# Kernel optimization log

Hardware: AMD Instinct MI355X
Metric: run time of the kernel (lower is better)

The kernel has to match this reference:

```python
import jax, jax.numpy as jnp
import numpy as np

B, H_, W_, C, HEADS, WS, SR = 4, 56, 56, 256, 8, 3, 4
HD = C // HEADS
N = H_ * W_
LL = WS * WS
PH, PW = H_ // SR, W_ // SR
PL = PH * PW
K_TAB = 2048


def _unfold3(x, H, W):
    # x: (B, C, H, W) -> (B, C, 9, H*W); matches torch nn.Unfold(kernel_size=3, padding=1)
    xp = jnp.pad(x, ((0, 0), (0, 0), (1, 1), (1, 1)))
    pats = jnp.stack([xp[:, :, i:i + H, j:j + W] for i in range(3) for j in range(3)], axis=2)
    return pats.reshape(x.shape[0], x.shape[1], 9, H * W)


def _l2n(x):
    # torch F.normalize(dim=-1) with eps=1e-12
    return x / jnp.maximum(jnp.linalg.norm(x, axis=-1, keepdims=True), 1e-12)


def setup_inputs() -> dict:
    key = jax.random.key(0)
    ks = jax.random.split(key, 24)
    x = jax.random.normal(ks[0], (B, N, C), jnp.float32)
    # padding mask from unfold of ones image (True where window element falls outside)
    ones = np.zeros((H_ + 2, W_ + 2), np.float32)
    ones[1:-1, 1:-1] = 1.0
    pats = np.stack([ones[i:i + H_, j:j + W_] for i in range(3) for j in range(3)], 0).reshape(9, N)
    padding_mask = jnp.asarray((pats == 0).T)  # (N, 9) bool
    local_valid = LL - padding_mask.sum(-1)
    seq_length_scale = jnp.log(local_valid.astype(jnp.float32) + PL)[:, None]  # (N,1)
    relative_pos_index = jax.random.randint(ks[1], (N * PL,), 0, K_TAB)
    relative_coords_table = jax.random.uniform(ks[2], (K_TAB, 2), jnp.float32, -1.0, 1.0)
    w = lambda k, shape: jax.random.normal(k, shape, jnp.float32) * 0.02
    inp = dict(
        x=x, H=H_, W=W_,
        relative_pos_index=relative_pos_index,
        relative_coords_table=relative_coords_table,
        seq_length_scale=seq_length_scale,
        padding_mask=padding_mask,
        q_w=w(ks[3], (C, C)), q_b=jnp.zeros((C,), jnp.float32),
        kv_w=w(ks[4], (2 * C, C)), kv_b=jnp.zeros((2 * C,), jnp.float32),
        sr_w=w(ks[5], (C, C)), sr_b=jnp.zeros((C,), jnp.float32),
        norm_g=jnp.ones((C,), jnp.float32), norm_b=jnp.zeros((C,), jnp.float32),
        cpb1_w=w(ks[6], (512, 2)), cpb1_b=jnp.zeros((512,), jnp.float32),
        cpb2_w=w(ks[7], (HEADS, 512)), cpb2_b=jnp.zeros((HEADS,), jnp.float32),
        temperature=jnp.log(jnp.exp(jnp.ones((HEADS, 1, 1), jnp.float32) / 0.24) - 1.0),
        query_embedding=w(ks[8], (HEADS, 1, HD)),
        rel_pos_bias_local=jax.random.normal(ks[9], (HEADS, LL), jnp.float32) * 0.0004,
        learnable_tokens=w(ks[10], (HEADS, HD, LL)),
        learnable_bias=jnp.zeros((HEADS, 1, LL), jnp.float32),
        proj_w=w(ks[11], (C, C)), proj_b=jnp.zeros((C,), jnp.float32),
    )
    return inp


def reference(x, H, W, relative_pos_index, relative_coords_table, seq_length_scale,
              padding_mask, q_w, q_b, kv_w, kv_b, sr_w, sr_b, norm_g, norm_b,
              cpb1_w, cpb1_b, cpb2_w, cpb2_b, temperature, query_embedding,
              rel_pos_bias_local, learnable_tokens, learnable_bias, proj_w, proj_b):
    Bsz, n, Cd = x.shape
    h, hd, ll = HEADS, HD, LL
    pH, pW = H // SR, W // SR
    pL = pH * pW
    # ----- queries -----
    q = (x @ q_w.T + q_b).reshape(Bsz, n, h, hd).transpose(0, 2, 1, 3)  # (B,h,N,d)
    q_norm = _l2n(q)
    q_scaled = (q_norm + query_embedding) * jax.nn.softplus(temperature) * seq_length_scale
    # ----- local branch: unfolded window KV -----
    kv = x @ kv_w.T + kv_b  # (B,N,2C)
    k_loc, v_loc = jnp.split(kv, 2, axis=-1)
    k_loc = _l2n(k_loc.reshape(Bsz, n, h, hd)).reshape(Bsz, n, Cd)
    kv_img = jnp.concatenate([k_loc, v_loc], -1).transpose(0, 2, 1).reshape(Bsz, 2 * Cd, H, W)
    pats = _unfold3(kv_img, H, W).reshape(Bsz, 2 * h, hd, ll, n).transpose(0, 1, 4, 2, 3)  # (B,2h,N,d,ll)
    k_local, v_local = jnp.split(pats, 2, axis=1)
    attn_local = jnp.einsum('bhnd,bhndl->bhnl', q_scaled, k_local) + rel_pos_bias_local[:, None, :]
    attn_local = jnp.where(padding_mask, -jnp.inf, attn_local)
    # ----- global branch: 1x1 conv -> GELU -> avg pool -> LN -> KV -----
    x_img = x.transpose(0, 2, 1).reshape(Bsz, Cd, H, W)
    x_sr = jax.nn.gelu(jnp.einsum('oc,bchw->bohw', sr_w, x_img) + sr_b[None, :, None, None], approximate=False)
    x_pool = x_sr.reshape(Bsz, Cd, pH, SR, pW, SR).mean(axis=(3, 5)).reshape(Bsz, Cd, pL).transpose(0, 2, 1)
    mu = x_pool.mean(-1, keepdims=True)
    var = x_pool.var(-1, keepdims=True)
    x_pool = (x_pool - mu) / jnp.sqrt(var + 1e-5) * norm_g + norm_b
    kvp = (x_pool @ kv_w.T + kv_b).reshape(Bsz, pL, 2 * h, hd).transpose(0, 2, 1, 3)
    k_pool, v_pool = jnp.split(kvp, 2, axis=1)  # each (B,h,pL,d)
    # CPB-MLP relative position bias (interpolate is identity since test==trained resolution)
    tab = jax.nn.relu(relative_coords_table @ cpb1_w.T + cpb1_b) @ cpb2_w.T + cpb2_b  # (K,h)
    pool_bias = tab.T[:, relative_pos_index].reshape(h, n, pL)
    attn_pool = jnp.einsum('bhnd,bhmd->bhnm', q_scaled, _l2n(k_pool)) + pool_bias
    # ----- joint softmax over [local | pool] -----
    attn = jax.nn.softmax(jnp.concatenate([attn_local, attn_pool], axis=-1), axis=-1)
    a_loc, a_pool = attn[..., :ll], attn[..., ll:]
    w_loc = jnp.einsum('bhnd,hdl->bhnl', q_norm, learnable_tokens) + learnable_bias + a_loc
    x_local = jnp.einsum('bhnl,bhndl->bhnd', w_loc, v_local)
    x_glob = jnp.einsum('bhnm,bhmd->bhnd', a_pool, v_pool)
    out = (x_local + x_glob).transpose(0, 2, 1, 3).reshape(Bsz, n, Cd)
    return out @ proj_w.T + proj_b
```

## Files before the change

### kernel.cpp

```cpp
#include <hip/hip_runtime.h>
#include <hip/hip_bf16.h>
#include <math.h>

#define Bn   4
#define Hh   56
#define Wn   56
#define Cn   256
#define NHn  8
#define HDn  32
#define Nn   3136
#define LLn  9
#define PLn  196
#define PWn  14
#define KTABn 2048
#define Mrows 12544
#define MP   224

#define XCNT   3211264
#define QWOFF  XCNT
#define KVWOFF (QWOFF + 65536)
#define SRWOFF (KVWOFF + 131072)
#define PWOFF  (SRWOFF + 65536)
#define TOTCVT (PWOFF + 65536)

typedef __attribute__((ext_vector_type(8))) short short8v;
typedef __attribute__((ext_vector_type(4))) float float4v;

__device__ __forceinline__ unsigned short f2b(float f) {
  __hip_bfloat16 h = __float2bfloat16(f);
  return *(unsigned short*)&h;
}
__device__ __forceinline__ float b2f(unsigned short u) {
  union { unsigned int i; float f; } x; x.i = ((unsigned int)u) << 16; return x.f;
}
__device__ __forceinline__ void u4_to8f(uint4 u, float* o) {
  o[0]=b2f((unsigned short)(u.x&0xffff)); o[1]=b2f((unsigned short)(u.x>>16));
  o[2]=b2f((unsigned short)(u.y&0xffff)); o[3]=b2f((unsigned short)(u.y>>16));
  o[4]=b2f((unsigned short)(u.z&0xffff)); o[5]=b2f((unsigned short)(u.z>>16));
  o[6]=b2f((unsigned short)(u.w&0xffff)); o[7]=b2f((unsigned short)(u.w>>16));
}

__launch_bounds__(256)
__global__ void cvt5(const float* __restrict__ x, const float* __restrict__ qw,
                     const float* __restrict__ kvw, const float* __restrict__ srw,
                     const float* __restrict__ pw, unsigned short* __restrict__ dst)
{
  const int i = (blockIdx.x * 256 + threadIdx.x) * 4;
  const float* src; int off;
  if      (i < XCNT)   { src = x;   off = 0; }
  else if (i < KVWOFF) { src = qw;  off = QWOFF; }
  else if (i < SRWOFF) { src = kvw; off = KVWOFF; }
  else if (i < PWOFF)  { src = srw; off = SRWOFF; }
  else                 { src = pw;  off = PWOFF; }
  const float4 v = *(const float4*)(src + (i - off));
  ushort4 o2;
  o2.x = f2b(v.x); o2.y = f2b(v.y); o2.z = f2b(v.z); o2.w = f2b(v.w);
  *(ushort4*)(dst + i) = o2;
}

template <int MODE>
__launch_bounds__(512)
__global__ void mgemm(const unsigned short* __restrict__ A,
                      const unsigned short* __restrict__ Wb,
                      const float* __restrict__ b0, const float* __restrict__ b1,
                      const float* __restrict__ b2, void* __restrict__ Cv, int Nc,
                      const float* __restrict__ sls, const float* __restrict__ qe,
                      const float* __restrict__ temp, float* __restrict__ Mq)
{
  __shared__ __align__(16) unsigned char smem[34816];
  unsigned short* As = (unsigned short*)smem;
  unsigned short* Bs = (unsigned short*)(smem + 16384);
  const int t = threadIdx.x;
  const int w = t >> 6, lane = t & 63;
  const int q = lane >> 4, ln = lane & 15;
  const int n0 = blockIdx.x * 128, m0 = blockIdx.y * 128;
  const int wm = (w >> 1) * 32, wn = (w & 1) * 64;

  float4v acc[2][4];
  #pragma unroll
  for (int mt = 0; mt < 2; ++mt)
    #pragma unroll
    for (int nt = 0; nt < 4; ++nt)
      acc[mt][nt] = (float4v){0.f, 0.f, 0.f, 0.f};

  for (int k0 = 0; k0 < 256; k0 += 64) {
    #pragma unroll
    for (int j = 0; j < 2; ++j) {
      const int u = t + 512 * j;
      const int r = u >> 3, cg = u & 7;
      const int cs = cg ^ (r & 7);
      const uint4 av = *(const uint4*)(A  + (size_t)(m0 + r) * 256 + k0 + cg * 8);
      *(uint4*)(As + r * 64 + cs * 8) = av;
      const uint4 bv = *(const uint4*)(Wb + (size_t)(n0 + r) * 256 + k0 + cg * 8);
      *(uint4*)(Bs + r * 64 + cs * 8) = bv;
    }
    __syncthreads();
    #pragma unroll
    for (int kk = 0; kk < 2; ++kk) {
      short8v af[2], bfr[4];
      const int cg = kk * 4 + q;
      #pragma unroll
      for (int mt = 0; mt < 2; ++mt) {
        const int r = wm + mt * 16 + ln;
        af[mt] = *(const short8v*)(As + r * 64 + (cg ^ (r & 7)) * 8);
      }
      #pragma unroll
      for (int nt = 0; nt < 4; ++nt) {
        const int r = wn + nt * 16 + ln;
        bfr[nt] = *(const short8v*)(Bs + r * 64 + (cg ^ (r & 7)) * 8);
      }
      #pragma unroll
      for (int mt = 0; mt < 2; ++mt)
        #pragma unroll
        for (int nt = 0; nt < 4; ++nt)
          acc[mt][nt] = __builtin_amdgcn_mfma_f32_16x16x32_bf16(af[mt], bfr[nt], acc[mt][nt], 0, 0, 0);
    }
    __syncthreads();
  }

  if constexpr (MODE == 0) {
    float* C = (float*)Cv;
    float* tileF = (float*)smem;
    float bia[4];
    #pragma unroll
    for (int nt = 0; nt < 4; ++nt) bia[nt] = b0[n0 + wn + nt * 16 + ln];
    #pragma unroll
    for (int half = 0; half < 2; ++half) {
      if ((w >> 2) == half) {
        #pragma unroll
        for (int mt = 0; mt < 2; ++mt)
          #pragma unroll
          for (int r = 0; r < 4; ++r)
            #pragma unroll
            for (int nt = 0; nt < 4; ++nt)
              tileF[(wm - half*64 + mt*16 + q*4 + r) * 132 + wn + nt*16 + ln] = acc[mt][nt][r] + bia[nt];
      }
      __syncthreads();
      #pragma unroll
      for (int j = 0; j < 4; ++j) {
        const int i = j * 512 + t;
        const int row = i >> 5, ch = i & 31;
        float4 v = *(const float4*)(tileF + row * 132 + ch * 4);
        *(float4*)(C + (size_t)(m0 + half * 64 + row) * Nc + n0 + ch * 4) = v;
      }
      __syncthreads();
    }
  } else {
    unsigned short* Cb = (unsigned short*)Cv;
    unsigned short* tileC = (unsigned short*)smem;
    const int seg = n0 >> 8;
    const int h0 = (n0 + wn) >> 5, h1 = h0 + 1;
    float spt0 = 0.f, spt1 = 0.f;
    if (seg == 0) { spt0 = log1pf(__expf(temp[h0])); spt1 = log1pf(__expf(temp[h1])); }
    float bia[4], qev[4];
    #pragma unroll
    for (int nt = 0; nt < 4; ++nt) {
      const int col = n0 + wn + nt * 16 + ln;
      bia[nt] = (seg == 0) ? b0[col] : (seg == 3 ? b2[col - 768] : b1[col - 256]);
      if (seg == 0) qev[nt] = qe[col];
    }
    #pragma unroll
    for (int mt = 0; mt < 2; ++mt) {
      #pragma unroll
      for (int r = 0; r < 4; ++r) {
        const int row = m0 + wm + mt * 16 + q * 4 + r;
        const int lrow = wm + mt * 16 + q * 4 + r;
        float vals[4];
        #pragma unroll
        for (int nt = 0; nt < 4; ++nt) vals[nt] = acc[mt][nt][r] + bia[nt];
        if (seg == 0) {
          float ss0 = vals[0]*vals[0] + vals[1]*vals[1];
          float ss1 = vals[2]*vals[2] + vals[3]*vals[3];
          #pragma unroll
          for (int mk = 1; mk <= 8; mk <<= 1) { ss0 += __shfl_xor(ss0, mk); ss1 += __shfl_xor(ss1, mk); }
          const float i0 = 1.f / fmaxf(sqrtf(ss0), 1e-12f);
          const float i1 = 1.f / fmaxf(sqrtf(ss1), 1e-12f);
          const int nidx = row % Nn, bb = row / Nn;
          const float sl = sls[nidx];
          float qsv[4];
          #pragma unroll
          for (int nt = 0; nt < 4; ++nt) {
            const float inv = (nt < 2) ? i0 : i1;
            const float sp  = (nt < 2) ? spt0 : spt1;
            qsv[nt] = (vals[nt] * inv + qev[nt]) * sp * sl;
          }
          float t0 = qsv[0]*qsv[0] + qsv[1]*qsv[1];
          float t1 = qsv[2]*qsv[2] + qsv[3]*qsv[3];
          #pragma unroll
          for (int mk = 1; mk <= 8; mk <<= 1) { t0 += __shfl_xor(t0, mk); t1 += __shfl_xor(t1, mk); }
          if (ln == 0) {
            Mq[((size_t)(bb * NHn + h0)) * Nn + nidx] = sqrtf(t0);
            Mq[((size_t)(bb * NHn + h1)) * Nn + nidx] = sqrtf(t1);
          }
          #pragma unroll
          for (int nt = 0; nt < 4; ++nt)
            tileC[lrow * 136 + wn + nt*16 + ln] = f2b(qsv[nt]);
        } else if (seg == 1) {
          float ss0 = vals[0]*vals[0] + vals[1]*vals[1];
          float ss1 = vals[2]*vals[2] + vals[3]*vals[3];
          #pragma unroll
          for (int mk = 1; mk <= 8; mk <<= 1) { ss0 += __shfl_xor(ss0, mk); ss1 += __shfl_xor(ss1, mk); }
          const float i0 = 1.f / fmaxf(sqrtf(ss0), 1e-12f);
          const float i1 = 1.f / fmaxf(sqrtf(ss1), 1e-12f);
          #pragma unroll
          for (int nt = 0; nt < 4; ++nt)
            tileC[lrow * 136 + wn + nt*16 + ln] = f2b(vals[nt] * ((nt < 2) ? i0 : i1));
        } else if (seg == 2) {
          #pragma unroll
          for (int nt = 0; nt < 4; ++nt)
            tileC[lrow * 136 + wn + nt*16 + ln] = f2b(vals[nt]);
        } else {
          #pragma unroll
          for (int nt = 0; nt < 4; ++nt) {
            const float v = vals[nt];
            tileC[lrow * 136 + wn + nt*16 + ln] =
              f2b(0.5f * v * (1.0f + erff(v * 0.70710678118654752f)));
          }
        }
      }
    }
    __syncthreads();
    #pragma unroll
    for (int j = 0; j < 4; ++j) {
      const int i = j * 512 + t;
      const int row = i >> 4, ch = i & 15;
      uint4 v = *(const uint4*)(tileC + row * 136 + ch * 8);
      *(uint4*)(Cb + (size_t)(m0 + row) * 1024 + n0 + ch * 8) = v;
    }
  }
}

__launch_bounds__(256)
__global__ void gemm_k(const float* __restrict__ A, const float* __restrict__ W,
                       const float* __restrict__ bias, float* __restrict__ Co,
                       int Mr, int Nc, int K)
{
  __shared__ __align__(16) float As[16][64];
  __shared__ __align__(16) float Ws[16][64];
  const int t  = threadIdx.x;
  const int m0 = blockIdx.y * 64, n0 = blockIdx.x * 64;
  const int lm = t >> 2, lk = (t & 3) << 2;
  const int tx = t & 15, ty = t >> 4;
  float acc[4][4] = {};
  int arow = m0 + lm; if (arow >= Mr) arow = Mr - 1;
  const int wrow = n0 + lm;
  for (int k0 = 0; k0 < K; k0 += 16) {
    float4 av = *(const float4*)(A + (size_t)arow * K + k0 + lk);
    As[lk+0][lm] = av.x; As[lk+1][lm] = av.y; As[lk+2][lm] = av.z; As[lk+3][lm] = av.w;
    float4 wv = *(const float4*)(W + (size_t)wrow * K + k0 + lk);
    Ws[lk+0][lm] = wv.x; Ws[lk+1][lm] = wv.y; Ws[lk+2][lm] = wv.z; Ws[lk+3][lm] = wv.w;
    __syncthreads();
    #pragma unroll
    for (int k = 0; k < 16; ++k) {
      float4 a = *(const float4*)&As[k][ty << 2];
      float4 w = *(const float4*)&Ws[k][tx << 2];
      acc[0][0] += a.x*w.x; acc[0][1] += a.x*w.y; acc[0][2] += a.x*w.z; acc[0][3] += a.x*w.w;
      acc[1][0] += a.y*w.x; acc[1][1] += a.y*w.y; acc[1][2] += a.y*w.z; acc[1][3] += a.y*w.w;
      acc[2][0] += a.z*w.x; acc[2][1] += a.z*w.y; acc[2][2] += a.z*w.z; acc[2][3] += a.z*w.w;
      acc[3][0] += a.w*w.x; acc[3][1] += a.w*w.y; acc[3][2] += a.w*w.z; acc[3][3] += a.w*w.w;
    }
    __syncthreads();
  }
  #pragma unroll
  for (int i = 0; i < 4; ++i) {
    const int row = m0 + (ty << 2) + i;
    if (row >= Mr) continue;
    #pragma unroll
    for (int j = 0; j < 4; ++j) {
      const int col = n0 + (tx << 2) + j;
      Co[(size_t)row * Nc + col] = acc[i][j] + bias[col];
    }
  }
}

__launch_bounds__(256)
__global__ void pool_ln_k(const unsigned short* __restrict__ fused, float* __restrict__ pln,
                          const float* __restrict__ g, const float* __restrict__ bb)
{
  const int blk = blockIdx.x;
  const int b = blk / PLn, pc = blk % PLn;
  const int pi = pc / PWn, pj = pc % PWn;
  const int c = threadIdx.x;
  float s = 0.f;
  #pragma unroll
  for (int r = 0; r < 4; ++r)
    #pragma unroll
    for (int cc = 0; cc < 4; ++cc) {
      const int n = (pi*4 + r) * Wn + pj*4 + cc;
      s += b2f(fused[((size_t)b * Nn + n) * 1024 + 768 + c]);
    }
  s *= (1.f/16.f);
  float sum = s, sq = s*s;
  #pragma unroll
  for (int m = 32; m >= 1; m >>= 1) { sum += __shfl_xor(sum, m); sq += __shfl_xor(sq, m); }
  __shared__ float sm[8];
  const int lane = c & 63, wid = c >> 6;
  if (lane == 0) { sm[wid] = sum; sm[4+wid] = sq; }
  __syncthreads();
  const float tot  = sm[0]+sm[1]+sm[2]+sm[3];
  const float totq = sm[4]+sm[5]+sm[6]+sm[7];
  const float mu  = tot * (1.f/256.f);
  const float var = totq * (1.f/256.f) - mu*mu;
  pln[(size_t)blk * Cn + c] = (s - mu) / sqrtf(var + 1e-5f) * g[c] + bb[c];
}

__launch_bounds__(256)
__global__ void pool_pack(const float* __restrict__ kvp, unsigned short* __restrict__ kbf,
                          unsigned short* __restrict__ vbf)
{
  const int bh = blockIdx.x;
  const int b = bh >> 3, h = bh & 7;
  const int t = threadIdx.x, mg = t >> 5, d = t & 31;
  for (int mi = 0; mi < MP/8; ++mi) {
    const int m = mi * 8 + mg;
    float kv2 = 0.f, vv = 0.f;
    if (m < PLn) {
      kv2 = kvp[((size_t)(b * PLn + m)) * 512 + h * HDn + d];
      vv  = kvp[((size_t)(b * PLn + m)) * 512 + 256 + h * HDn + d];
    }
    float ssn = kv2 * kv2;
    #pragma unroll
    for (int mm = 16; mm >= 1; mm >>= 1) ssn += __shfl_xor(ssn, mm);
    const float kn = (m < PLn) ? kv2 / fmaxf(sqrtf(ssn), 1e-12f) : 0.f;
    kbf[((size_t)bh * MP + m) * HDn + d] = f2b(kn);
    vbf[((size_t)bh * 32 + d) * MP + m] = f2b(vv);
  }
}

__launch_bounds__(64)
__global__ void cpb_k(const float* __restrict__ rct, const float* __restrict__ w1,
                      const float* __restrict__ b1, const float* __restrict__ w2,
                      const float* __restrict__ b2, float* __restrict__ tab)
{
  const int r = blockIdx.x, t = threadIdx.x;
  const float c0 = rct[r*2], c1 = rct[r*2+1];
  float part[8] = {};
  #pragma unroll
  for (int jj = 0; jj < 8; ++jj) {
    const int j = t * 8 + jj;
    float hv = fmaxf(c0 * w1[j*2] + c1 * w1[j*2+1] + b1[j], 0.f);
    #pragma unroll
    for (int h = 0; h < 8; ++h) part[h] += hv * w2[h*512 + j];
  }
  #pragma unroll
  for (int h = 0; h < 8; ++h)
    for (int mm = 32; mm >= 1; mm >>= 1) part[h] += __shfl_xor(part[h], mm);
  if (t < 8) tab[r*8 + t] = part[t] + b2[t];
}

__launch_bounds__(256)
__global__ void redmax_k(const float* __restrict__ tab, const float* __restrict__ rpb,
                         float* __restrict__ scal)
{
  float mx = -1e30f;
  for (int i = threadIdx.x; i < KTABn*NHn; i += 256) mx = fmaxf(mx, tab[i]);
  if (threadIdx.x < NHn*LLn) mx = fmaxf(mx, rpb[threadIdx.x]);
  #pragma unroll
  for (int m = 32; m >= 1; m >>= 1) mx = fmaxf(mx, __shfl_xor(mx, m));
  __shared__ float sm[4];
  if ((threadIdx.x & 63) == 0) sm[threadIdx.x >> 6] = mx;
  __syncthreads();
  if (threadIdx.x == 0) scal[0] = fmaxf(fmaxf(sm[0], sm[1]), fmaxf(sm[2], sm[3]));
}

__launch_bounds__(256)
__global__ void bias_g2(const int* __restrict__ rpi, const float* __restrict__ tab,
                        unsigned short* __restrict__ bias2)
{
  const int tid = blockIdx.x * 256 + threadIdx.x;
  const int n = tid / MP, m = tid - n * MP;
  if (m < PLn) {
    const int idx = rpi[(size_t)n * PLn + m];
    #pragma unroll
    for (int h = 0; h < NHn; ++h)
      bias2[((size_t)h * Nn + n) * MP + m] = f2b(tab[(size_t)idx * NHn + h]);
  } else {
    #pragma unroll
    for (int h = 0; h < NHn; ++h)
      bias2[((size_t)h * Nn + n) * MP + m] = 0xFF80;
  }
}

__launch_bounds__(256)
__global__ void attn_f(const unsigned short* __restrict__ fused,
                       const unsigned short* __restrict__ kbf,
                       const unsigned short* __restrict__ vbf,
                       const unsigned short* __restrict__ bias2,
                       const float* __restrict__ Mq, const float* __restrict__ scal,
                       const float* __restrict__ slsp, const float* __restrict__ temp,
                       const float* __restrict__ qe, const float* __restrict__ lt,
                       const float* __restrict__ lb, const float* __restrict__ rpb,
                       unsigned short* __restrict__ outp)
{
  __shared__ __align__(16) unsigned short sh[7488];
  unsigned short* p_lds = sh;
  float* park = (float*)(sh + 2560);
  float* tabf = park + 2112;
  float* qe_s  = tabf;
  float* lt_s  = tabf + 32;
  float* lb_s  = tabf + 320;
  float* rpb_s = tabf + 329;
  const int t = threadIdx.x;
  const int w = t >> 6, lane = t & 63;
  const int ln = lane & 15, quad = lane >> 4;
  const int tile = blockIdx.x, h = blockIdx.y, b = blockIdx.z;
  const int bh = b * NHn + h;

  if (t < 32) qe_s[t] = qe[h * HDn + t];
  for (int i = t; i < HDn * LLn; i += 256) lt_s[i] = lt[h * HDn * LLn + i];
  if (t < LLn) { lb_s[t] = lb[h * LLn + t]; rpb_s[t] = rpb[h * LLn + t]; }
  __syncthreads();

  const int nb = tile * 64 + w * 16;
  const short8v afrag = *(const short8v*)(fused +
      ((size_t)(b * Nn + nb + ln)) * 1024 + h * HDn + quad * 8);
  float M4[4];
  const float sc = scal[0];
  #pragma unroll
  for (int r = 0; r < 4; ++r) M4[r] = Mq[(size_t)bh * Nn + nb + quad * 4 + r] + sc;

  const unsigned short* kg = kbf + (size_t)bh * (MP * HDn);
  const unsigned short* vg = vbf + (size_t)bh * (32 * MP);
  unsigned short* pst = p_lds + w * 640;

  float4v accO[2];
  accO[0] = (float4v){0.f,0.f,0.f,0.f};
  accO[1] = (float4v){0.f,0.f,0.f,0.f};
  float lsum[4] = {0.f, 0.f, 0.f, 0.f};

  #pragma unroll
  for (int kc = 0; kc < 7; ++kc) {
    #pragma unroll
    for (int mtl = 0; mtl < 2; ++mtl) {
      const int mt = kc * 2 + mtl;
      short8v bfrag = *(const short8v*)(kg + (mt * 16 + ln) * HDn + quad * 8);
      float4v s = __builtin_amdgcn_mfma_f32_16x16x32_bf16(afrag, bfrag,
                                                          (float4v){0.f,0.f,0.f,0.f}, 0, 0, 0);
      #pragma unroll
      for (int r = 0; r < 4; ++r) {
        const int nr = nb + quad * 4 + r;
        const float bv = b2f(bias2[((size_t)h * Nn + nr) * MP + mt * 16 + ln]);
        const float p = __expf(s[r] + bv - M4[r]);
        const unsigned short pb = f2b(p);
        lsum[r] += b2f(pb);
        pst[(quad * 4 + r) * 40 + mtl * 16 + ln] = pb;
      }
    }
    short8v pa = *(const short8v*)(pst + ln * 40 + quad * 8);
    #pragma unroll
    for (int nt = 0; nt < 2; ++nt) {
      short8v vb = *(const short8v*)(vg + (size_t)(nt * 16 + ln) * MP + kc * 32 + quad * 8);
      accO[nt] = __builtin_amdgcn_mfma_f32_16x16x32_bf16(pa, vb, accO[nt], 0, 0, 0);
    }
  }

  #pragma unroll
  for (int r = 0; r < 4; ++r) {
    #pragma unroll
    for (int mk = 1; mk <= 8; mk <<= 1) lsum[r] += __shfl_xor(lsum[r], mk);
  }

  float* mypark = park + w * 528;
  #pragma unroll
  for (int r = 0; r < 4; ++r) {
    const int row = quad * 4 + r;
    mypark[row * 33 + ln]      = accO[0][r];
    mypark[row * 33 + 16 + ln] = accO[1][r];
    if (ln == 0) mypark[row * 33 + 32] = lsum[r];
  }

  const int nl = t >> 2, dg = t & 3;
  const int n = tile * 64 + nl;
  const unsigned short* qp = fused + ((size_t)(b * Nn + n)) * 1024 + h * HDn + dg * 8;
  float qs8[8];
  u4_to8f(*(const uint4*)qp, qs8);
  const float M = Mq[(size_t)bh * Nn + n] + sc;
  const float spt = log1pf(__expf(temp[h]));
  const float inv_qs = 1.f / (spt * slsp[n]);

  float acc8[8], ext8[8];
  #pragma unroll
  for (int j = 0; j < 8; ++j) { acc8[j] = 0.f; ext8[j] = 0.f; }
  float l_run = 0.f;
  const int pi = n / Wn, pj = n % Wn;
  #pragma unroll
  for (int lc = 0; lc < LLn; ++lc) {
    const int ii = pi + lc/3 - 1, jj = pj + (lc%3) - 1;
    if (ii < 0 || ii >= Hh || jj < 0 || jj >= Wn) continue;
    const int nb2 = ii * Wn + jj;
    const unsigned short* kr = fused + ((size_t)(b * Nn + nb2)) * 1024 + 256 + h * HDn + dg * 8;
    float kk8[8], vv8[8];
    u4_to8f(*(const uint4*)kr, kk8);
    u4_to8f(*(const uint4*)(kr + 256), vv8);
    float pp = 0.f, ep = 0.f;
    #pragma unroll
    for (int j = 0; j < 8; ++j) {
      pp += qs8[j] * kk8[j];
      ep += (qs8[j] * inv_qs - qe_s[dg*8 + j]) * lt_s[(dg*8 + j) * LLn + lc];
    }
    pp += __shfl_xor(pp, 1); pp += __shfl_xor(pp, 2);
    ep += __shfl_xor(ep, 1); ep += __shfl_xor(ep, 2);
    const float e = ep + lb_s[lc];
    const float p = __expf(pp + rpb_s[lc] - M);
    l_run += p;
    #pragma unroll
    for (int j = 0; j < 8; ++j) { acc8[j] += p * vv8[j]; ext8[j] += e * vv8[j]; }
  }

  const float* pool_r = park + w * 528 + (nl - w * 16) * 33;
  const float l_pool = pool_r[32];
  const float invl = 1.f / (l_run + l_pool);
  uint4 u;
  {
    const float* op = pool_r + dg * 8;
    float o0 = (acc8[0]+op[0])*invl + ext8[0], o1 = (acc8[1]+op[1])*invl + ext8[1];
    float o2 = (acc8[2]+op[2])*invl + ext8[2], o3 = (acc8[3]+op[3])*invl + ext8[3];
    float o4 = (acc8[4]+op[4])*invl + ext8[4], o5 = (acc8[5]+op[5])*invl + ext8[5];
    float o6 = (acc8[6]+op[6])*invl + ext8[6], o7 = (acc8[7]+op[7])*invl + ext8[7];
    u.x = f2b(o0) | ((unsigned int)f2b(o1) << 16);
    u.y = f2b(o2) | ((unsigned int)f2b(o3) << 16);
    u.z = f2b(o4) | ((unsigned int)f2b(o5) << 16);
    u.w = f2b(o6) | ((unsigned int)f2b(o7) << 16);
  }
  *(uint4*)(outp + ((size_t)b * Nn + n) * Cn + h * HDn + dg * 8) = u;
}

extern "C" void kernel_launch(void* const* d_in, const int* in_sizes, int n_in,
                              void* d_out, int out_size, void* d_ws, size_t ws_size,
                              hipStream_t stream)
{
  const float* x    = (const float*)d_in[0];
  const int*   rpi  = (const int*)d_in[3];
  const float* rct  = (const float*)d_in[4];
  const float* sls  = (const float*)d_in[5];
  const float* q_w  = (const float*)d_in[7];
  const float* q_b  = (const float*)d_in[8];
  const float* kv_w = (const float*)d_in[9];
  const float* kv_b = (const float*)d_in[10];
  const float* sr_w = (const float*)d_in[11];
  const float* sr_b = (const float*)d_in[12];
  const float* ng   = (const float*)d_in[13];
  const float* nbta = (const float*)d_in[14];
  const float* c1w  = (const float*)d_in[15];
  const float* c1b  = (const float*)d_in[16];
  const float* c2w  = (const float*)d_in[17];
  const float* c2b  = (const float*)d_in[18];
  const float* temp = (const float*)d_in[19];
  const float* qe   = (const float*)d_in[20];
  const float* rpb  = (const float*)d_in[21];
  const float* lt   = (const float*)d_in[22];
  const float* lb   = (const float*)d_in[23];
  const float* pw   = (const float*)d_in[24];
  const float* pb   = (const float*)d_in[25];

  float* ws = (float*)d_ws;
  size_t o = 0;
  unsigned short* bf = (unsigned short*)(ws + o); o += TOTCVT / 2;
  unsigned short* fused = (unsigned short*)(ws + o); o += (size_t)Mrows * 512;
  float* Mq    = ws + o;  o += (size_t)Bn * NHn * Nn;
  float* pln   = ws + o;  o += (size_t)Bn * PLn * Cn;
  float* kvp   = ws + o;  o += (size_t)Bn * PLn * 2 * Cn;
  unsigned short* kbf = (unsigned short*)(ws + o); o += (size_t)Bn * NHn * MP * HDn / 2;
  unsigned short* vbf = (unsigned short*)(ws + o); o += (size_t)Bn * NHn * 32 * MP / 2;
  float* tab   = ws + o;  o += (size_t)KTABn * NHn;
  float* scal  = ws + o;  o += 8;
  unsigned short* bias2 = (unsigned short*)(ws + o); o += (size_t)NHn * Nn * MP / 2;
  unsigned short* outp  = (unsigned short*)(ws + o); o += (size_t)Mrows * Cn / 2;

  const unsigned short* xbf   = bf;
  const unsigned short* qkvsw = bf + QWOFF;
  const unsigned short* pwbf  = bf + PWOFF;

  cvt5<<<TOTCVT/1024, 256, 0, stream>>>(x, q_w, kv_w, sr_w, pw, bf);
  mgemm<1><<<dim3(8, 98), 512, 0, stream>>>(xbf, qkvsw, q_b, kv_b, sr_b, fused, 1024,
                                            sls, qe, temp, Mq);
  pool_ln_k<<<Bn*PLn, 256, 0, stream>>>(fused, pln, ng, nbta);
  gemm_k<<<dim3(8, 13), 256, 0, stream>>>(pln, kv_w, kv_b, kvp, Bn*PLn, 512, 256);
  pool_pack<<<Bn*NHn, 256, 0, stream>>>(kvp, kbf, vbf);
  cpb_k<<<KTABn, 64, 0, stream>>>(rct, c1w, c1b, c2w, c2b, tab);
  redmax_k<<<1, 256, 0, stream>>>(tab, rpb, scal);
  bias_g2<<<(Nn*MP)/256, 256, 0, stream>>>(rpi, tab, bias2);
  attn_f<<<dim3(49, NHn, Bn), 256, 0, stream>>>(fused, kbf, vbf, bias2, Mq, scal,
                                                sls, temp, qe, lt, lb, rpb, outp);
  mgemm<0><<<dim3(2, 98), 512, 0, stream>>>(outp, pwbf, pb, pb, pb, (float*)d_out, 256,
                                            nullptr, nullptr, nullptr, nullptr);
}
```

Before: 251.7 us.

## Write q/k/v from QKV GEMM into per-head planar layout for attention

The fused QKV GEMM epilogue now writes the q, k and v segments into separate head-major planes (B*heads, N, head_dim) instead of the interleaved 1024-wide row layout. Only the fourth segment, which pool_ln_k still reads, keeps the old layout. The attention kernel reads q, local k and local v from these planes, so each head's data is contiguous and neighbour loads touch less scattered memory. The cost is a different, more scattered store pattern in the GEMM epilogue and extra workspace.

```diff
diff --git a/kernel.cpp b/kernel.cpp
--- a/kernel.cpp
+++ b/kernel.cpp
@@ -15,6 +15,7 @@
 #define KTABn 2048
 #define Mrows 12544
 #define MP   224
+#define PLSZ (Bn*NHn*Nn*HDn)
 
 #define XCNT   3211264
 #define QWOFF  XCNT
@@ -65,7 +66,8 @@
                       const float* __restrict__ b0, const float* __restrict__ b1,
                       const float* __restrict__ b2, void* __restrict__ Cv, int Nc,
                       const float* __restrict__ sls, const float* __restrict__ qe,
-                      const float* __restrict__ temp, float* __restrict__ Mq)
+                      const float* __restrict__ temp, float* __restrict__ Mq,
+                      unsigned short* __restrict__ planes)
 {
   __shared__ __align__(16) unsigned char smem[34816];
   unsigned short* As = (unsigned short*)smem;
@@ -220,12 +222,26 @@
       }
     }
     __syncthreads();
-    #pragma unroll
-    for (int j = 0; j < 4; ++j) {
-      const int i = j * 512 + t;
-      const int row = i >> 4, ch = i & 15;
-      uint4 v = *(const uint4*)(tileC + row * 136 + ch * 8);
-      *(uint4*)(Cb + (size_t)(m0 + row) * 1024 + n0 + ch * 8) = v;
+    if (seg == 3) {
+      #pragma unroll
+      for (int j = 0; j < 4; ++j) {
+        const int i = j * 512 + t;
+        const int row = i >> 4, ch = i & 15;
+        uint4 v = *(const uint4*)(tileC + row * 136 + ch * 8);
+        *(uint4*)(Cb + (size_t)(m0 + row) * 1024 + n0 + ch * 8) = v;
+      }
+    } else {
+      unsigned short* plane = planes + (size_t)seg * PLSZ;
+      const int hbase = (n0 & 255) >> 5;
+      const int row = t >> 2, c4 = t & 3;
+      const int grow = m0 + row;
+      const int bb2 = grow / Nn, nidx = grow - bb2 * Nn;
+      #pragma unroll
+      for (int j = 0; j < 4; ++j) {
+        uint4 v = *(const uint4*)(tileC + row * 136 + (j * 4 + c4) * 8);
+        const int bh2 = bb2 * NHn + hbase + j;
+        *(uint4*)(plane + ((size_t)bh2 * Nn + nidx) * HDn + c4 * 8) = v;
+      }
     }
   }
 }
@@ -382,7 +398,9 @@
 }
 
 __launch_bounds__(256)
-__global__ void attn_f(const unsigned short* __restrict__ fused,
+__global__ void attn_f(const unsigned short* __restrict__ qloc,
+                       const unsigned short* __restrict__ kloc,
+                       const unsigned short* __restrict__ vloc,
                        const unsigned short* __restrict__ kbf,
                        const unsigned short* __restrict__ vbf,
                        const unsigned short* __restrict__ bias2,
@@ -411,9 +429,12 @@
   if (t < LLn) { lb_s[t] = lb[h * LLn + t]; rpb_s[t] = rpb[h * LLn + t]; }
   __syncthreads();
 
+  const unsigned short* qpl = qloc + (size_t)bh * Nn * HDn;
+  const unsigned short* kpl = kloc + (size_t)bh * Nn * HDn;
+  const unsigned short* vpl = vloc + (size_t)bh * Nn * HDn;
+
   const int nb = tile * 64 + w * 16;
-  const short8v afrag = *(const short8v*)(fused +
-      ((size_t)(b * Nn + nb + ln)) * 1024 + h * HDn + quad * 8);
+  const short8v afrag = *(const short8v*)(qpl + (size_t)(nb + ln) * HDn + quad * 8);
   float M4[4];
   const float sc = scal[0];
   #pragma unroll
@@ -471,9 +492,8 @@
 
   const int nl = t >> 2, dg = t & 3;
   const int n = tile * 64 + nl;
-  const unsigned short* qp = fused + ((size_t)(b * Nn + n)) * 1024 + h * HDn + dg * 8;
   float qs8[8];
-  u4_to8f(*(const uint4*)qp, qs8);
+  u4_to8f(*(const uint4*)(qpl + (size_t)n * HDn + dg * 8), qs8);
   const float M = Mq[(size_t)bh * Nn + n] + sc;
   const float spt = log1pf(__expf(temp[h]));
   const float inv_qs = 1.f / (spt * slsp[n]);
@@ -488,10 +508,9 @@
     const int ii = pi + lc/3 - 1, jj = pj + (lc%3) - 1;
     if (ii < 0 || ii >= Hh || jj < 0 || jj >= Wn) continue;
     const int nb2 = ii * Wn + jj;
-    const unsigned short* kr = fused + ((size_t)(b * Nn + nb2)) * 1024 + 256 + h * HDn + dg * 8;
     float kk8[8], vv8[8];
-    u4_to8f(*(const uint4*)kr, kk8);
-    u4_to8f(*(const uint4*)(kr + 256), vv8);
+    u4_to8f(*(const uint4*)(kpl + (size_t)nb2 * HDn + dg * 8), kk8);
+    u4_to8f(*(const uint4*)(vpl + (size_t)nb2 * HDn + dg * 8), vv8);
     float pp = 0.f, ep = 0.f;
     #pragma unroll
     for (int j = 0; j < 8; ++j) {
@@ -566,6 +585,10 @@
   float* scal  = ws + o;  o += 8;
   unsigned short* bias2 = (unsigned short*)(ws + o); o += (size_t)NHn * Nn * MP / 2;
   unsigned short* outp  = (unsigned short*)(ws + o); o += (size_t)Mrows * Cn / 2;
+  unsigned short* qkv3  = (unsigned short*)(ws + o); o += 3 * (size_t)PLSZ / 2;
+  unsigned short* qloc = qkv3;
+  unsigned short* klocp = qkv3 + PLSZ;
+  unsigned short* vlocp = qkv3 + 2 * (size_t)PLSZ;
 
   const unsigned short* xbf   = bf;
   const unsigned short* qkvsw = bf + QWOFF;
@@ -573,15 +596,15 @@
 
   cvt5<<<TOTCVT/1024, 256, 0, stream>>>(x, q_w, kv_w, sr_w, pw, bf);
   mgemm<1><<<dim3(8, 98), 512, 0, stream>>>(xbf, qkvsw, q_b, kv_b, sr_b, fused, 1024,
-                                            sls, qe, temp, Mq);
+                                            sls, qe, temp, Mq, qkv3);
   pool_ln_k<<<Bn*PLn, 256, 0, stream>>>(fused, pln, ng, nbta);
   gemm_k<<<dim3(8, 13), 256, 0, stream>>>(pln, kv_w, kv_b, kvp, Bn*PLn, 512, 256);
   pool_pack<<<Bn*NHn, 256, 0, stream>>>(kvp, kbf, vbf);
   cpb_k<<<KTABn, 64, 0, stream>>>(rct, c1w, c1b, c2w, c2b, tab);
   redmax_k<<<1, 256, 0, stream>>>(tab, rpb, scal);
   bias_g2<<<(Nn*MP)/256, 256, 0, stream>>>(rpi, tab, bias2);
-  attn_f<<<dim3(49, NHn, Bn), 256, 0, stream>>>(fused, kbf, vbf, bias2, Mq, scal,
-                                                sls, temp, qe, lt, lb, rpb, outp);
+  attn_f<<<dim3(49, NHn, Bn), 256, 0, stream>>>(qloc, klocp, vlocp, kbf, vbf, bias2,
+                                                Mq, scal, sls, temp, qe, lt, lb, rpb, outp);
   mgemm<0><<<dim3(2, 98), 512, 0, stream>>>(outp, pwbf, pb, pb, pb, (float*)d_out, 256,
-                                            nullptr, nullptr, nullptr, nullptr);
-}
+                                            nullptr, nullptr, nullptr, nullptr, nullptr);
+}
```

New measurement: 268.5 us. 6.7% more time.

## Tile pool bias layout for MFMA reads and stage local K/V halo in LDS

Applied to the files above, without the earlier changes.

The pooled-attention bias is stored in 16x16 tiles matching the MFMA output fragment, so each wave reads its bias as contiguous 256-element chunks instead of strided rows. The attention kernel also preloads a halo of local keys and values (64 rows plus neighbour rows) into shared memory once per block, replacing nine repeated global gathers per query. This raises LDS use per block, which may lower occupancy, and the clamped halo indices depend on the boundary checks that follow.

```diff
diff --git a/kernel.cpp b/kernel.cpp
--- a/kernel.cpp
+++ b/kernel.cpp
@@ -367,18 +367,22 @@
 __global__ void bias_g2(const int* __restrict__ rpi, const float* __restrict__ tab,
                         unsigned short* __restrict__ bias2)
 {
-  const int tid = blockIdx.x * 256 + threadIdx.x;
-  const int n = tid / MP, m = tid - n * MP;
+  const int mt = blockIdx.x, nt = blockIdx.y;
+  const int t = threadIdx.x;
+  const int nn = t >> 4, mm = t & 15;
+  const int n = nt * 16 + nn, m = mt * 16 + mm;
+  unsigned short vh[NHn];
   if (m < PLn) {
     const int idx = rpi[(size_t)n * PLn + m];
     #pragma unroll
-    for (int h = 0; h < NHn; ++h)
-      bias2[((size_t)h * Nn + n) * MP + m] = f2b(tab[(size_t)idx * NHn + h]);
+    for (int h = 0; h < NHn; ++h) vh[h] = f2b(tab[(size_t)idx * NHn + h]);
   } else {
     #pragma unroll
-    for (int h = 0; h < NHn; ++h)
-      bias2[((size_t)h * Nn + n) * MP + m] = 0xFF80;
-  }
+    for (int h = 0; h < NHn; ++h) vh[h] = 0xFF80;
+  }
+  #pragma unroll
+  for (int h = 0; h < NHn; ++h)
+    bias2[(((size_t)h * 196 + nt) * 14 + mt) * 256 + t] = vh[h];
 }
 
 __launch_bounds__(256)
@@ -392,10 +396,12 @@
                        const float* __restrict__ lb, const float* __restrict__ rpb,
                        unsigned short* __restrict__ outp)
 {
-  __shared__ __align__(16) unsigned short sh[7488];
-  unsigned short* p_lds = sh;
-  float* park = (float*)(sh + 2560);
-  float* tabf = park + 2112;
+  __shared__ __align__(16) unsigned short sh[21888];
+  unsigned short* k_s   = sh;
+  unsigned short* v_s   = sh + 7200;
+  unsigned short* p_lds = sh + 14400;
+  float* park = (float*)(sh + 16960);
+  float* tabf = (float*)(sh + 21184);
   float* qe_s  = tabf;
   float* lt_s  = tabf + 32;
   float* lb_s  = tabf + 320;
@@ -409,6 +415,14 @@
   if (t < 32) qe_s[t] = qe[h * HDn + t];
   for (int i = t; i < HDn * LLn; i += 256) lt_s[i] = lt[h * HDn * LLn + i];
   if (t < LLn) { lb_s[t] = lb[h * LLn + t]; rpb_s[t] = rpb[h * LLn + t]; }
+  const int base_n = tile * 64 - 57;
+  for (int i = t; i < 720; i += 256) {
+    const int row = i >> 2, c4 = i & 3;
+    int rg = base_n + row; rg = rg < 0 ? 0 : (rg > Nn - 1 ? Nn - 1 : rg);
+    const unsigned short* src = fused + ((size_t)(b * Nn + rg)) * 1024 + 256 + h * HDn + c4 * 8;
+    *(uint4*)(k_s + row * 40 + c4 * 8) = *(const uint4*)src;
+    *(uint4*)(v_s + row * 40 + c4 * 8) = *(const uint4*)(src + 256);
+  }
   __syncthreads();
 
   const int nb = tile * 64 + w * 16;
@@ -421,6 +435,7 @@
 
   const unsigned short* kg = kbf + (size_t)bh * (MP * HDn);
   const unsigned short* vg = vbf + (size_t)bh * (32 * MP);
+  const unsigned short* b2t = bias2 + (((size_t)h * 196 + (tile * 4 + w)) * 14) * 256;
   unsigned short* pst = p_lds + w * 640;
 
   float4v accO[2];
@@ -438,8 +453,7 @@
                                                           (float4v){0.f,0.f,0.f,0.f}, 0, 0, 0);
       #pragma unroll
       for (int r = 0; r < 4; ++r) {
-        const int nr = nb + quad * 4 + r;
-        const float bv = b2f(bias2[((size_t)h * Nn + nr) * MP + mt * 16 + ln]);
+        const float bv = b2f(b2t[mt * 256 + (quad * 4 + r) * 16 + ln]);
         const float p = __expf(s[r] + bv - M4[r]);
         const unsigned short pb = f2b(p);
         lsum[r] += b2f(pb);
@@ -471,9 +485,8 @@
 
   const int nl = t >> 2, dg = t & 3;
   const int n = tile * 64 + nl;
-  const unsigned short* qp = fused + ((size_t)(b * Nn + n)) * 1024 + h * HDn + dg * 8;
   float qs8[8];
-  u4_to8f(*(const uint4*)qp, qs8);
+  u4_to8f(*(const uint4*)(fused + ((size_t)(b * Nn + n)) * 1024 + h * HDn + dg * 8), qs8);
   const float M = Mq[(size_t)bh * Nn + n] + sc;
   const float spt = log1pf(__expf(temp[h]));
   const float inv_qs = 1.f / (spt * slsp[n]);
@@ -483,15 +496,15 @@
   for (int j = 0; j < 8; ++j) { acc8[j] = 0.f; ext8[j] = 0.f; }
   float l_run = 0.f;
   const int pi = n / Wn, pj = n % Wn;
+  const int sb = nl + 57;
   #pragma unroll
   for (int lc = 0; lc < LLn; ++lc) {
     const int ii = pi + lc/3 - 1, jj = pj + (lc%3) - 1;
     if (ii < 0 || ii >= Hh || jj < 0 || jj >= Wn) continue;
-    const int nb2 = ii * Wn + jj;
-    const unsigned short* kr = fused + ((size_t)(b * Nn + nb2)) * 1024 + 256 + h * HDn + dg * 8;
+    const int slot = sb + (lc/3 - 1) * 56 + (lc%3) - 1;
     float kk8[8], vv8[8];
-    u4_to8f(*(const uint4*)kr, kk8);
-    u4_to8f(*(const uint4*)(kr + 256), vv8);
+    u4_to8f(*(const uint4*)(k_s + slot * 40 + dg * 8), kk8);
+    u4_to8f(*(const uint4*)(v_s + slot * 40 + dg * 8), vv8);
     float pp = 0.f, ep = 0.f;
     #pragma unroll
     for (int j = 0; j < 8; ++j) {
@@ -579,7 +592,7 @@
   pool_pack<<<Bn*NHn, 256, 0, stream>>>(kvp, kbf, vbf);
   cpb_k<<<KTABn, 64, 0, stream>>>(rct, c1w, c1b, c2w, c2b, tab);
   redmax_k<<<1, 256, 0, stream>>>(tab, rpb, scal);
-  bias_g2<<<(Nn*MP)/256, 256, 0, stream>>>(rpi, tab, bias2);
+  bias_g2<<<dim3(14, 196), 256, 0, stream>>>(rpi, tab, bias2);
   attn_f<<<dim3(49, NHn, Bn), 256, 0, stream>>>(fused, kbf, vbf, bias2, Mq, scal,
                                                 sls, temp, qe, lt, lb, rpb, outp);
   mgemm<0><<<dim3(2, 98), 512, 0, stream>>>(outp, pwbf, pb, pb, pb, (float*)d_out, 256,
```

New measurement: 251.2 us. Within noise of the previous version (-0.2%).
